# Kernel optimization log

Hardware: AMD Instinct MI355X
Metric: run time of the kernel (lower is better)

Reference implementation:

```python
import jax, jax.numpy as jnp
import numpy as np

FLTRSTDEV = 2.0
EXTGRADFAC = 10.0
DMAX = 15.0
ENHANCEMENT = 2.0   # enhancement_factor in the module
NEG_WEIGHT = 1.5    # negative_weight in the module


def make_gauss_edge_fltr(stdev: float) -> np.ndarray:
    """Gaussian-derivative edge filter, shape [2, 1, k, k] (OIHW), k = 2*ceil(2*stdev)+1."""
    r = int(np.ceil(2.0 * stdev))
    x = np.arange(-r, r + 1, dtype=np.float32)
    g = np.exp(-x ** 2 / (2.0 * stdev ** 2)).astype(np.float32)
    g /= g.sum()
    dg = (-x / (stdev ** 2)) * np.exp(-x ** 2 / (2.0 * stdev ** 2))
    dg = (dg / np.abs(dg).sum()).astype(np.float32)
    f_dy = np.outer(dg, g)   # gradient along axis 0
    f_dx = np.outer(g, dg)   # gradient along axis 1
    return np.stack([f_dy, f_dx])[:, None]  # [2,1,k,k]


def cmpt_grad_im(img, fltr):
    """img: [B,1,H,W], fltr: [2,1,k,k] -> [B,2,H,W] gradient image (SAME conv)."""
    return jax.lax.conv_general_dilated(
        img, fltr, window_strides=(1, 1), padding='SAME',
        dimension_numbers=('NCHW', 'OIHW', 'NCHW'))


def setup_inputs() -> dict:
    key = jax.random.key(0)
    k1, k2 = jax.random.split(key)
    B, H, W = 16, 1024, 1024
    # predicted signed distance map, roughly in [-DMAX, DMAX]
    pred_dmap = jax.random.normal(k1, (B, 1, H, W), dtype=jnp.float32) * 5.0
    # stand-in for the snake-rendered signed distance map (detached target)
    snake_dm = jax.random.normal(k2, (B, 1, H, W), dtype=jnp.float32) * 5.0
    fltr = jnp.asarray(make_gauss_edge_fltr(FLTRSTDEV))
    return {"pred_dmap": pred_dmap, "snake_dm": snake_dm, "fltr": fltr}


def reference(pred_dmap, snake_dm, fltr):
    # external-energy gradient images driving the snakes
    gimg = cmpt_grad_im(pred_dmap, fltr) * EXTGRADFAC           # [B,2,H,W]
    gimgW = cmpt_grad_im(jnp.abs(pred_dmap), fltr) * EXTGRADFAC  # [B,2,H,W]
    # dmap[dmap > 0] = dmax  (background set to +dmax)
    sd = jnp.where(snake_dm > 0, DMAX, snake_dm)
    # snake_dm[snake_dm < 0] *= enhancement_factor
    sd = jnp.where(sd < 0, sd * ENHANCEMENT, sd)
    neg_mask = (sd < 0).astype(pred_dmap.dtype)
    squared_diff = (pred_dmap - jax.lax.stop_gradient(sd)) ** 2
    loss = jnp.mean(squared_diff * (1.0 + neg_mask * NEG_WEIGHT))
    return loss, gimg, gimgW
```

## Files before the change

### kernel.cpp

```cpp
#include <hip/hip_runtime.h>

#define HH 1024
#define WW 1024
#define BB 16
#define RR 4
#define TY 32
#define TX 64
#define LW (TX + 8)
#define DMAXC 15.0f
#define ENHC 2.0f
#define NEGWC 1.5f
#define EGFC 10.0f

__device__ __forceinline__ void fma4(float4& a, float c, const float4& v) {
    a.x += c * v.x; a.y += c * v.y; a.z += c * v.z; a.w += c * v.w;
}

__device__ __forceinline__ float4 hconv(const float* __restrict__ row, int xg,
                                        const float (&cf)[9]) {
    float w[12];
    *(float4*)&w[0] = *(const float4*)&row[xg];
    *(float4*)&w[4] = *(const float4*)&row[xg + 4];
    *(float4*)&w[8] = *(const float4*)&row[xg + 8];
    float4 acc = make_float4(0.f, 0.f, 0.f, 0.f);
#pragma unroll
    for (int j = 0; j < 9; ++j) {
        float c = cf[j];
        acc.x += c * w[j];
        acc.y += c * w[j + 1];
        acc.z += c * w[j + 2];
        acc.w += c * w[j + 3];
    }
    return acc;
}

__device__ __forceinline__ float lossterm(float p, float s) {
    float sd = (s > 0.f) ? DMAXC : s;
    sd = (sd < 0.f) ? sd * ENHC : sd;
    float w = (sd < 0.f) ? (1.f + NEGWC) : 1.f;
    float d = p - sd;
    return d * d * w;
}

__global__ __launch_bounds__(256) void snake_fused(
    const float* __restrict__ pred, const float* __restrict__ snake,
    const float* __restrict__ fltr, float* __restrict__ out) {
    __shared__ float s_in[(TY + 8) * LW];
    __shared__ float s_vA[TY * LW];
    __shared__ float s_vB[TY * LW];
    __shared__ float s_wA[TY * LW];
    __shared__ float s_wB[TY * LW];
    __shared__ float s_dg[9];
    __shared__ float s_g[9];
    __shared__ float s_red[4];

    const int t = threadIdx.x;
    const int gx0 = blockIdx.x * TX;
    const int gy0 = blockIdx.y * TY;
    const int b = blockIdx.z;
    const float* img = pred + (size_t)b * (HH * WW);

    if (t < 9) {
        float s = 0.f;
#pragma unroll
        for (int j = 0; j < 9; ++j) s += fltr[t * 9 + j];
        s_dg[t] = s;
    }
    __syncthreads();
    if (t < 9) s_g[t] = fltr[t] / s_dg[0];

    for (int idx = t; idx < (TY + 8) * LW; idx += 256) {
        int yy = idx / LW;
        int xx = idx - yy * LW;
        int gy = gy0 + yy - RR;
        int gx = gx0 + xx - RR;
        float v = 0.f;
        if ((unsigned)gy < HH && (unsigned)gx < WW) v = img[(size_t)gy * WW + gx];
        s_in[idx] = v;
    }
    __syncthreads();

    float dgr[9], gr[9];
#pragma unroll
    for (int i = 0; i < 9; ++i) { dgr[i] = s_dg[i]; gr[i] = s_g[i]; }

    for (int gidx = t; gidx < TY * (LW / 4); gidx += 256) {
        int y = gidx / (LW / 4);
        int xg = (gidx - y * (LW / 4)) * 4;
        float4 a = make_float4(0.f, 0.f, 0.f, 0.f);
        float4 bb = a, wa = a, wb = a;
#pragma unroll
        for (int i = 0; i < 9; ++i) {
            float4 v = *(const float4*)&s_in[(y + i) * LW + xg];
            float4 av = make_float4(fabsf(v.x), fabsf(v.y), fabsf(v.z), fabsf(v.w));
            fma4(a, dgr[i], v);
            fma4(bb, gr[i], v);
            fma4(wa, dgr[i], av);
            fma4(wb, gr[i], av);
        }
        *(float4*)&s_vA[y * LW + xg] = a;
        *(float4*)&s_vB[y * LW + xg] = bb;
        *(float4*)&s_wA[y * LW + xg] = wa;
        *(float4*)&s_wB[y * LW + xg] = wb;
    }
    __syncthreads();

    float lsum = 0.f;
    float* gimg = out + 1;
    float* gimgW = out + 1 + (size_t)BB * 2 * HH * WW;
    const float* snk = snake + (size_t)b * (HH * WW);

    for (int gidx = t; gidx < TY * (TX / 4); gidx += 256) {
        int y = gidx >> 4;
        int xg = (gidx & 15) * 4;
        const int ro = y * LW;
        float4 dy = hconv(&s_vA[ro], xg, gr);
        float4 dx = hconv(&s_vB[ro], xg, dgr);
        float4 dyW = hconv(&s_wA[ro], xg, gr);
        float4 dxW = hconv(&s_wB[ro], xg, dgr);

        int gy = gy0 + y, gx = gx0 + xg;
        size_t p0 = ((size_t)(b * 2 + 0)) * (HH * WW) + (size_t)gy * WW + gx;
        size_t p1 = ((size_t)(b * 2 + 1)) * (HH * WW) + (size_t)gy * WW + gx;
        gimg[p0 + 0] = EGFC * dy.x;  gimg[p0 + 1] = EGFC * dy.y;
        gimg[p0 + 2] = EGFC * dy.z;  gimg[p0 + 3] = EGFC * dy.w;
        gimg[p1 + 0] = EGFC * dx.x;  gimg[p1 + 1] = EGFC * dx.y;
        gimg[p1 + 2] = EGFC * dx.z;  gimg[p1 + 3] = EGFC * dx.w;
        gimgW[p0 + 0] = EGFC * dyW.x; gimgW[p0 + 1] = EGFC * dyW.y;
        gimgW[p0 + 2] = EGFC * dyW.z; gimgW[p0 + 3] = EGFC * dyW.w;
        gimgW[p1 + 0] = EGFC * dxW.x; gimgW[p1 + 1] = EGFC * dxW.y;
        gimgW[p1 + 2] = EGFC * dxW.z; gimgW[p1 + 3] = EGFC * dxW.w;

        float4 pv = *(const float4*)&s_in[(y + RR) * LW + xg + RR];
        float4 sv = *(const float4*)&snk[(size_t)gy * WW + gx];
        lsum += lossterm(pv.x, sv.x) + lossterm(pv.y, sv.y) +
                lossterm(pv.z, sv.z) + lossterm(pv.w, sv.w);
    }

#pragma unroll
    for (int off = 32; off > 0; off >>= 1) lsum += __shfl_down(lsum, off);
    if ((t & 63) == 0) s_red[t >> 6] = lsum;
    __syncthreads();
    if (t == 0) {
        float tot = s_red[0] + s_red[1] + s_red[2] + s_red[3];
        atomicAdd(out, tot * (1.0f / 16777216.0f));
    }
}

extern "C" void kernel_launch(void* const* d_in, const int* in_sizes, int n_in,
                              void* d_out, int out_size, void* d_ws, size_t ws_size,
                              hipStream_t stream) {
    const float* pred = (const float*)d_in[0];
    const float* snake = (const float*)d_in[1];
    const float* fltr = (const float*)d_in[2];
    float* out = (float*)d_out;

    hipMemsetAsync(out, 0, sizeof(float), stream);

    dim3 grid(WW / TX, HH / TY, BB);
    snake_fused<<<grid, 256, 0, stream>>>(pred, snake, fltr, out);
}
```

Before: 476.0 us.

## Stream rows per wavefront with register ring buffer for separable convolution

Replaces the 2D shared-memory tile, which needed an 8-row vertical halo, with a per-wavefront row-streaming scheme. Each wave owns 64 columns and walks 64 rows, computing the horizontal passes into a 9-entry register ring and emitting the vertical pass each row. This cuts the halo overhead from 40/32 to 72/64 rows, removes the large LDS buffers and block-wide barriers, and writes outputs with coalesced per-lane scalar stores. In exchange it uses many more registers for the ring buffers, which may lower occupancy, and each wave does serial row-by-row loads with only a wave-local LDS exchange.

```diff
diff --git a/kernel.cpp b/kernel.cpp
--- a/kernel.cpp
+++ b/kernel.cpp
@@ -3,36 +3,11 @@
 #define HH 1024
 #define WW 1024
 #define BB 16
-#define RR 4
-#define TY 32
-#define TX 64
-#define LW (TX + 8)
+#define ROWS 64
 #define DMAXC 15.0f
 #define ENHC 2.0f
 #define NEGWC 1.5f
 #define EGFC 10.0f
-
-__device__ __forceinline__ void fma4(float4& a, float c, const float4& v) {
-    a.x += c * v.x; a.y += c * v.y; a.z += c * v.z; a.w += c * v.w;
-}
-
-__device__ __forceinline__ float4 hconv(const float* __restrict__ row, int xg,
-                                        const float (&cf)[9]) {
-    float w[12];
-    *(float4*)&w[0] = *(const float4*)&row[xg];
-    *(float4*)&w[4] = *(const float4*)&row[xg + 4];
-    *(float4*)&w[8] = *(const float4*)&row[xg + 8];
-    float4 acc = make_float4(0.f, 0.f, 0.f, 0.f);
-#pragma unroll
-    for (int j = 0; j < 9; ++j) {
-        float c = cf[j];
-        acc.x += c * w[j];
-        acc.y += c * w[j + 1];
-        acc.z += c * w[j + 2];
-        acc.w += c * w[j + 3];
-    }
-    return acc;
-}
 
 __device__ __forceinline__ float lossterm(float p, float s) {
     float sd = (s > 0.f) ? DMAXC : s;
@@ -42,104 +17,116 @@
     return d * d * w;
 }
 
-__global__ __launch_bounds__(256) void snake_fused(
+__device__ __forceinline__ float rfl(float x) {
+    return __uint_as_float(__builtin_amdgcn_readfirstlane(__float_as_uint(x)));
+}
+
+#define HROW(SLOT, YIN, DOLOSS)                                               \
+    {                                                                         \
+        const int yin_ = (YIN);                                               \
+        if (lane < 18) {                                                      \
+            int gc_ = c0 - 4 + 4 * lane;                                      \
+            float4 v_ = make_float4(0.f, 0.f, 0.f, 0.f);                      \
+            if ((unsigned)yin_ < HH && (unsigned)gc_ < WW)                    \
+                v_ = *(const float4*)&img[(size_t)yin_ * WW + gc_];           \
+            *(float4*)&s_row[wid][4 * lane] = v_;                             \
+        }                                                                     \
+        asm volatile("s_waitcnt lgkmcnt(0)" ::: "memory");                    \
+        float wv_[9];                                                         \
+        _Pragma("unroll")                                                     \
+        for (int k_ = 0; k_ < 9; ++k_) wv_[k_] = s_row[wid][lane + k_];       \
+        float hg_ = 0.f, hd_ = 0.f, ag_ = 0.f, ad_ = 0.f;                     \
+        _Pragma("unroll")                                                     \
+        for (int k_ = 0; k_ < 9; ++k_) {                                      \
+            float v_ = wv_[k_];                                               \
+            float a_ = fabsf(v_);                                             \
+            hg_ += g[k_] * v_;                                                \
+            hd_ += dg[k_] * v_;                                               \
+            ag_ += g[k_] * a_;                                                \
+            ad_ += dg[k_] * a_;                                               \
+        }                                                                     \
+        hgP[SLOT] = hg_; hdP[SLOT] = hd_;                                     \
+        hgA[SLOT] = ag_; hdA[SLOT] = ad_;                                     \
+        if (DOLOSS) {                                                         \
+            float sv_ = snk[(size_t)yin_ * WW + c0 + lane];                   \
+            lsum += lossterm(wv_[4], sv_);                                    \
+        }                                                                     \
+    }
+
+#define EMIT(YO, BASE)                                                        \
+    {                                                                         \
+        float c0_ = 0.f, c1_ = 0.f, w0_ = 0.f, w1_ = 0.f;                     \
+        _Pragma("unroll")                                                     \
+        for (int i_ = 0; i_ < 9; ++i_) {                                      \
+            const int s_ = ((BASE) + i_) % 9;            \
+            c0_ += dg[i_] * hgP[s_];                                          \
+            c1_ += g[i_] * hdP[s_];                                           \
+            w0_ += dg[i_] * hgA[s_];                                          \
+            w1_ += g[i_] * hdA[s_];                                           \
+        }                                                                     \
+        size_t o_ = (size_t)(YO) * WW + c0 + lane;                            \
+        g0[o_] = EGFC * c0_;                                                  \
+        g1[o_] = EGFC * c1_;                                                  \
+        g0W[o_] = EGFC * w0_;                                                 \
+        g1W[o_] = EGFC * w1_;                                                 \
+    }
+
+__global__ __launch_bounds__(256) void snake_rows(
     const float* __restrict__ pred, const float* __restrict__ snake,
-    const float* __restrict__ fltr, float* __restrict__ out) {
-    __shared__ float s_in[(TY + 8) * LW];
-    __shared__ float s_vA[TY * LW];
-    __shared__ float s_vB[TY * LW];
-    __shared__ float s_wA[TY * LW];
-    __shared__ float s_wB[TY * LW];
-    __shared__ float s_dg[9];
-    __shared__ float s_g[9];
+    const float* __restrict__ fltr, float* __restrict__ out)
+{
+    __shared__ float s_row[4][72];
     __shared__ float s_red[4];
 
     const int t = threadIdx.x;
-    const int gx0 = blockIdx.x * TX;
-    const int gy0 = blockIdx.y * TY;
+    const int lane = t & 63;
+    const int wid = t >> 6;
     const int b = blockIdx.z;
-    const float* img = pred + (size_t)b * (HH * WW);
+    const int r0 = blockIdx.y * ROWS;
+    const int c0 = blockIdx.x * 256 + wid * 64;
 
-    if (t < 9) {
+    float g[9], dg[9];
+#pragma unroll
+    for (int i = 0; i < 9; ++i) {
         float s = 0.f;
 #pragma unroll
-        for (int j = 0; j < 9; ++j) s += fltr[t * 9 + j];
-        s_dg[t] = s;
+        for (int j = 0; j < 9; ++j) s += fltr[i * 9 + j];
+        dg[i] = rfl(s);
     }
-    __syncthreads();
-    if (t < 9) s_g[t] = fltr[t] / s_dg[0];
+    {
+        float inv = 1.f / dg[0];
+#pragma unroll
+        for (int j = 0; j < 9; ++j) g[j] = rfl(fltr[j] * inv);
+    }
 
-    for (int idx = t; idx < (TY + 8) * LW; idx += 256) {
-        int yy = idx / LW;
-        int xx = idx - yy * LW;
-        int gy = gy0 + yy - RR;
-        int gx = gx0 + xx - RR;
-        float v = 0.f;
-        if ((unsigned)gy < HH && (unsigned)gx < WW) v = img[(size_t)gy * WW + gx];
-        s_in[idx] = v;
+    const float* img = pred + (size_t)b * (HH * WW);
+    const float* snk = snake + (size_t)b * (HH * WW);
+    float* g0 = out + 1 + ((size_t)(b * 2 + 0)) * (HH * WW);
+    float* g1 = out + 1 + ((size_t)(b * 2 + 1)) * (HH * WW);
+    float* g0W = g0 + (size_t)BB * 2 * HH * WW;
+    float* g1W = g1 + (size_t)BB * 2 * HH * WW;
+
+    float hgP[9], hdP[9], hgA[9], hdA[9];
+    float lsum = 0.f;
+
+    #pragma unroll
+    for (int j = 0; j < 9; ++j) {
+        HROW(j, r0 - 4 + j, j >= 4);
     }
-    __syncthreads();
+    EMIT(r0, 0);
 
-    float dgr[9], gr[9];
+    for (int jj = 9; jj < 72; jj += 9) {
 #pragma unroll
-    for (int i = 0; i < 9; ++i) { dgr[i] = s_dg[i]; gr[i] = s_g[i]; }
-
-    for (int gidx = t; gidx < TY * (LW / 4); gidx += 256) {
-        int y = gidx / (LW / 4);
-        int xg = (gidx - y * (LW / 4)) * 4;
-        float4 a = make_float4(0.f, 0.f, 0.f, 0.f);
-        float4 bb = a, wa = a, wb = a;
-#pragma unroll
-        for (int i = 0; i < 9; ++i) {
-            float4 v = *(const float4*)&s_in[(y + i) * LW + xg];
-            float4 av = make_float4(fabsf(v.x), fabsf(v.y), fabsf(v.z), fabsf(v.w));
-            fma4(a, dgr[i], v);
-            fma4(bb, gr[i], v);
-            fma4(wa, dgr[i], av);
-            fma4(wb, gr[i], av);
+        for (int u = 0; u < 9; ++u) {
+            const int j = jj + u;
+            HROW(u, r0 - 4 + j, j < 68);
+            EMIT(r0 + j - 8, (u + 1) % 9);
         }
-        *(float4*)&s_vA[y * LW + xg] = a;
-        *(float4*)&s_vB[y * LW + xg] = bb;
-        *(float4*)&s_wA[y * LW + xg] = wa;
-        *(float4*)&s_wB[y * LW + xg] = wb;
-    }
-    __syncthreads();
-
-    float lsum = 0.f;
-    float* gimg = out + 1;
-    float* gimgW = out + 1 + (size_t)BB * 2 * HH * WW;
-    const float* snk = snake + (size_t)b * (HH * WW);
-
-    for (int gidx = t; gidx < TY * (TX / 4); gidx += 256) {
-        int y = gidx >> 4;
-        int xg = (gidx & 15) * 4;
-        const int ro = y * LW;
-        float4 dy = hconv(&s_vA[ro], xg, gr);
-        float4 dx = hconv(&s_vB[ro], xg, dgr);
-        float4 dyW = hconv(&s_wA[ro], xg, gr);
-        float4 dxW = hconv(&s_wB[ro], xg, dgr);
-
-        int gy = gy0 + y, gx = gx0 + xg;
-        size_t p0 = ((size_t)(b * 2 + 0)) * (HH * WW) + (size_t)gy * WW + gx;
-        size_t p1 = ((size_t)(b * 2 + 1)) * (HH * WW) + (size_t)gy * WW + gx;
-        gimg[p0 + 0] = EGFC * dy.x;  gimg[p0 + 1] = EGFC * dy.y;
-        gimg[p0 + 2] = EGFC * dy.z;  gimg[p0 + 3] = EGFC * dy.w;
-        gimg[p1 + 0] = EGFC * dx.x;  gimg[p1 + 1] = EGFC * dx.y;
-        gimg[p1 + 2] = EGFC * dx.z;  gimg[p1 + 3] = EGFC * dx.w;
-        gimgW[p0 + 0] = EGFC * dyW.x; gimgW[p0 + 1] = EGFC * dyW.y;
-        gimgW[p0 + 2] = EGFC * dyW.z; gimgW[p0 + 3] = EGFC * dyW.w;
-        gimgW[p1 + 0] = EGFC * dxW.x; gimgW[p1 + 1] = EGFC * dxW.y;
-        gimgW[p1 + 2] = EGFC * dxW.z; gimgW[p1 + 3] = EGFC * dxW.w;
-
-        float4 pv = *(const float4*)&s_in[(y + RR) * LW + xg + RR];
-        float4 sv = *(const float4*)&snk[(size_t)gy * WW + gx];
-        lsum += lossterm(pv.x, sv.x) + lossterm(pv.y, sv.y) +
-                lossterm(pv.z, sv.z) + lossterm(pv.w, sv.w);
     }
 
 #pragma unroll
     for (int off = 32; off > 0; off >>= 1) lsum += __shfl_down(lsum, off);
-    if ((t & 63) == 0) s_red[t >> 6] = lsum;
+    if (lane == 0) s_red[wid] = lsum;
     __syncthreads();
     if (t == 0) {
         float tot = s_red[0] + s_red[1] + s_red[2] + s_red[3];
@@ -157,6 +144,6 @@
 
     hipMemsetAsync(out, 0, sizeof(float), stream);
 
-    dim3 grid(WW / TX, HH / TY, BB);
-    snake_fused<<<grid, 256, 0, stream>>>(pred, snake, fltr, out);
+    dim3 grid(WW / 256, HH / ROWS, BB);
+    snake_rows<<<grid, 256, 0, stream>>>(pred, snake, fltr, out);
 }
```

New measurement: 416.8 us. 12.4% less time.
